# Performance work log

Hardware: AMD Instinct MI355X
Metric: run time of the kernel (lower is better)

The kernel has to match this reference:

```python
import jax, jax.numpy as jnp
import numpy as np


def setup_inputs() -> dict:
    key = jax.random.key(0)
    k1, k2, k3, k4 = jax.random.split(key, 4)
    B, H, W, C = 4, 64, 64, 512
    x = jax.random.normal(k1, (B, H, W, C), dtype=jnp.float32)
    Wb = jax.random.normal(k2, (C, C // 8), dtype=jnp.float32) * 0.05
    Wc = jax.random.normal(k3, (C, C // 8), dtype=jnp.float32) * 0.05
    Wd = jax.random.normal(k4, (C, C), dtype=jnp.float32) * 0.05
    gamma = jnp.ones((1,), dtype=jnp.float32)
    return {"x": x, "Wb": Wb, "Wc": Wc, "Wd": Wd, "gamma": gamma}


def reference(x, Wb, Wc, Wd, gamma):
    B, H, W, C = x.shape
    hw = H * W
    xf = x.reshape(B, hw, C)                      # [B, hw, C]
    b = jnp.einsum('bnc,ck->bnk', xf, Wb)         # key   [B, hw, C/8]
    c = jnp.einsum('bnc,ck->bnk', xf, Wc)         # query [B, hw, C/8]
    d = jnp.einsum('bnc,cf->bnf', xf, Wd)         # value [B, hw, C]
    # attention energy: c @ b^T, softmax over last axis (keras default)
    energy = jnp.einsum('bqk,bnk->bqn', c, b)     # [B, hw, hw]
    attn = jax.nn.softmax(energy, axis=-1)
    out = jnp.einsum('bqn,bnf->bqf', attn, d)     # [B, hw, C]
    out = out.reshape(B, H, W, C)
    return gamma * out + x
```

## Files before the change

kernel.cpp:

```cpp
#include <hip/hip_runtime.h>
#include <hip/hip_bf16.h>
#include <stdint.h>

typedef __attribute__((ext_vector_type(8))) short short8;
typedef __attribute__((ext_vector_type(4))) float f32x4;
typedef _Float16 half8 __attribute__((ext_vector_type(8)));

#define LOG2E 1.4426950408889634f
#define SHIFT2 100.98865286222744f

__device__ __forceinline__ unsigned short f2bf(float f) {
  union { float f; unsigned u; } v; v.f = f;
  unsigned u = v.u;
  unsigned r = u + 0x7FFF + ((u >> 16) & 1);
  return (unsigned short)(r >> 16);
}
__device__ __forceinline__ float bf2f(unsigned short h) {
  union { unsigned u; float f; } v; v.u = ((unsigned)h) << 16; return v.f;
}

__global__ void convert_x_kernel(const float* __restrict__ x,
                                 unsigned short* __restrict__ xh,
                                 _Float16* __restrict__ xf, int n4) {
  int i = blockIdx.x * blockDim.x + threadIdx.x;
  if (i >= n4) return;
  float4 v = ((const float4*)x)[i];
  ushort4 h;
  h.x = f2bf(v.x); h.y = f2bf(v.y); h.z = f2bf(v.z); h.w = f2bf(v.w);
  union { _Float16 f[4]; ushort4 u; } p;
  p.f[0] = (_Float16)v.x; p.f[1] = (_Float16)v.y;
  p.f[2] = (_Float16)v.z; p.f[3] = (_Float16)v.w;
  ((ushort4*)xh)[i] = h;
  ((ushort4*)xf)[i] = p.u;
}

__global__ void prep_w_kernel(const float* __restrict__ Wb,
                              const float* __restrict__ Wc,
                              const float* __restrict__ Wd,
                              _Float16* __restrict__ wf,
                              unsigned short* __restrict__ whd) {
  int gid = blockIdx.x * 256 + threadIdx.x;
  int n = gid >> 9, k = gid & 511;
  if (n < 128) {
    float v = (n < 64) ? Wb[k * 64 + n] : Wc[k * 64 + (n - 64)];
    wf[n * 512 + k] = (_Float16)v;
  } else {
    whd[(size_t)(n - 128) * 512 + k] = f2bf(Wd[k * 512 + (n - 128)]);
  }
}

__launch_bounds__(256)
__global__ void proj_gemm_kernel(const unsigned short* __restrict__ xh,
                                 const _Float16* __restrict__ xf,
                                 const unsigned short* __restrict__ whd,
                                 const _Float16* __restrict__ wf,
                                 _Float16* __restrict__ bq,
                                 _Float16* __restrict__ cq,
                                 unsigned short* __restrict__ dT) {
  __shared__ unsigned short As[128 * 32];
  __shared__ unsigned short Bs[128 * 32];
  const int row0 = blockIdx.x * 128;
  const int col0 = blockIdx.y * 128;
  const bool bc = (blockIdx.y == 0);
  const int w = threadIdx.x >> 6;
  const int lane = threadIdx.x & 63;
  const int wm = (w >> 1) * 64, wn = (w & 1) * 64;
  const int quad = lane >> 4, m16 = lane & 15;
  const int lrow = lane >> 2, lseg = lane & 3;

  const unsigned short* asrc = bc ? (const unsigned short*)xf : xh;
  const unsigned short* bsrc = bc ? (const unsigned short*)wf : whd;
  const int bcol0 = bc ? 0 : (col0 - 128);

  const f32x4 fzero = {0.f, 0.f, 0.f, 0.f};
  f32x4 acc[4][4];
  for (int i = 0; i < 4; i++)
    for (int j = 0; j < 4; j++) acc[i][j] = fzero;

  for (int k0 = 0; k0 < 512; k0 += 32) {
    for (int i = 0; i < 2; i++) {
      int r = (w * 2 + i) * 16 + lrow;
      size_t aoff = (size_t)(row0 + r) * 512 + k0 + lseg * 8;
      size_t boff = (size_t)(bcol0 + r) * 512 + k0 + lseg * 8;
      int loff = r * 32 + lseg * 8;
      __builtin_amdgcn_global_load_lds(
          (const __attribute__((address_space(1))) unsigned int*)(asrc + aoff),
          (__attribute__((address_space(3))) unsigned int*)(As + loff), 16, 0, 0);
      __builtin_amdgcn_global_load_lds(
          (const __attribute__((address_space(1))) unsigned int*)(bsrc + boff),
          (__attribute__((address_space(3))) unsigned int*)(Bs + loff), 16, 0, 0);
    }
    __syncthreads();
    if (bc) {
      half8 ah[4], bh[4];
      for (int mt = 0; mt < 4; mt++)
        ah[mt] = *(const half8*)(As + (wm + mt * 16 + m16) * 32 + quad * 8);
      for (int nt = 0; nt < 4; nt++)
        bh[nt] = *(const half8*)(Bs + (wn + nt * 16 + m16) * 32 + quad * 8);
      for (int mt = 0; mt < 4; mt++)
        for (int nt = 0; nt < 4; nt++)
          acc[mt][nt] = __builtin_amdgcn_mfma_f32_16x16x32_f16(ah[mt], bh[nt],
                                                               acc[mt][nt], 0, 0, 0);
    } else {
      short8 ah[4], bh[4];
      for (int mt = 0; mt < 4; mt++)
        ah[mt] = *(const short8*)(As + (wm + mt * 16 + m16) * 32 + quad * 8);
      for (int nt = 0; nt < 4; nt++)
        bh[nt] = *(const short8*)(Bs + (wn + nt * 16 + m16) * 32 + quad * 8);
      for (int mt = 0; mt < 4; mt++)
        for (int nt = 0; nt < 4; nt++)
          acc[mt][nt] = __builtin_amdgcn_mfma_f32_16x16x32_bf16(ah[mt], bh[nt],
                                                                acc[mt][nt], 0, 0, 0);
    }
    __syncthreads();
  }

  for (int mt = 0; mt < 4; mt++) {
    int rowb = row0 + wm + mt * 16 + quad * 4;
    for (int nt = 0; nt < 4; nt++) {
      int n = wn + nt * 16 + m16;
      f32x4 v = acc[mt][nt];
      if (bc) {
        _Float16* dst = (n < 64) ? bq : cq;
        int nn = n & 63;
        for (int r = 0; r < 4; r++)
          dst[(size_t)(rowb + r) * 64 + nn] = (_Float16)v[r];
      } else {
        int f = col0 - 128 + n;
        int batch = rowb >> 12, tok = rowb & 4095;
        ushort4 o;
        o.x = f2bf(v[0]); o.y = f2bf(v[1]); o.z = f2bf(v[2]); o.w = f2bf(v[3]);
        *(ushort4*)(dT + ((size_t)batch * 512 + f) * 4096 + tok) = o;
      }
    }
  }
}

#define PSTR 72

__launch_bounds__(256, 2)
__global__ void attn_kernel(const _Float16* __restrict__ bq,
                            const _Float16* __restrict__ cq,
                            const unsigned short* __restrict__ dT,
                            float* __restrict__ O0,
                            float* __restrict__ O1,
                            float* __restrict__ lbuf) {
  __shared__ unsigned short p_lds[2][64 * PSTR];

  const int batch = blockIdx.y;
  const int split = blockIdx.z;
  const int q0 = blockIdx.x * 64;
  const int tid = threadIdx.x;
  const int w = tid >> 6, lane = tid & 63;
  const int quad = lane >> 4, m16 = lane & 15;
  const int colc = w * 16 + m16;

  const _Float16* cb = cq + ((size_t)batch * 4096 + q0) * 64;
  const _Float16* kb = bq + (size_t)batch * 4096 * 64;
  const unsigned short* vb = dT + (size_t)batch * 512 * 4096;
  float* Op = split ? O1 : O0;

  half8 qf[4][2];
  for (int mt = 0; mt < 4; mt++)
    for (int ks = 0; ks < 2; ks++)
      qf[mt][ks] = *(const half8*)(cb + (size_t)(mt * 16 + m16) * 64 +
                                   ks * 32 + quad * 8);

  const f32x4 fzero = {0.f, 0.f, 0.f, 0.f};
  f32x4 acc[4][8];
  for (int i = 0; i < 4; i++)
    for (int j = 0; j < 8; j++) acc[i][j] = fzero;

  const int sq = tid >> 2, sseg = tid & 3;
  float psum = 0.0f;

  const int kt0 = split * 32, kt1 = kt0 + 32;

  auto qk_step = [&](int kti, int nbuf) {
    const _Float16* kp = kb + ((size_t)kti * 64 + colc) * 64 + quad * 8;
    half8 K0 = *(const half8*)(kp);
    half8 K1 = *(const half8*)(kp + 32);
    for (int mt = 0; mt < 4; mt++) {
      f32x4 s = __builtin_amdgcn_mfma_f32_16x16x32_f16(qf[mt][0], K0, fzero, 0, 0, 0);
      s = __builtin_amdgcn_mfma_f32_16x16x32_f16(qf[mt][1], K1, s, 0, 0, 0);
      int rbase = mt * 16 + quad * 4;
#pragma unroll
      for (int r = 0; r < 4; r++) {
        float p = __builtin_amdgcn_exp2f(fmaf(s[r], LOG2E, -SHIFT2));
        p_lds[nbuf][(rbase + r) * PSTR + colc] = f2bf(p);
      }
    }
  };

  qk_step(kt0, 0);
  __syncthreads();

  for (int kt = kt0; kt < kt1; kt++) {
    const int buf = kt & 1;

    short8 vf0[8];
#pragma unroll
    for (int ft = 0; ft < 8; ft++)
      vf0[ft] = *(const short8*)(vb + (size_t)(w * 128 + ft * 16 + m16) * 4096 +
                                 kt * 64 + quad * 8);

    if (kt + 1 < kt1) qk_step(kt + 1, buf ^ 1);

    short8 vf1[8];
#pragma unroll
    for (int ft = 0; ft < 8; ft++)
      vf1[ft] = *(const short8*)(vb + (size_t)(w * 128 + ft * 16 + m16) * 4096 +
                                 kt * 64 + 32 + quad * 8);

    {
      const unsigned short* pr = p_lds[buf] + sq * PSTR + sseg * 16;
      short8 a = *(const short8*)(pr);
      short8 b = *(const short8*)(pr + 8);
      float ps = 0.f;
#pragma unroll
      for (int i = 0; i < 8; i++)
        ps += bf2f((unsigned short)a[i]) + bf2f((unsigned short)b[i]);
      psum += ps;
    }

    for (int ks = 0; ks < 2; ks++) {
      short8 pf[4];
      for (int mt = 0; mt < 4; mt++)
        pf[mt] = *(const short8*)(p_lds[buf] + (mt * 16 + m16) * PSTR +
                                  ks * 32 + quad * 8);
      const short8* vv = ks ? vf1 : vf0;
      for (int ft = 0; ft < 8; ft++)
        for (int mt = 0; mt < 4; mt++)
          acc[mt][ft] = __builtin_amdgcn_mfma_f32_16x16x32_bf16(pf[mt], vv[ft],
                                                                acc[mt][ft], 0, 0, 0);
    }
    __syncthreads();
  }

  psum += __shfl_xor(psum, 1);
  psum += __shfl_xor(psum, 2);
  if (sseg == 0)
    lbuf[(size_t)split * 16384 + batch * 4096 + (q0 + sq)] = psum;
  for (int mt = 0; mt < 4; mt++) {
    for (int ft = 0; ft < 8; ft++) {
      int f = w * 128 + ft * 16 + m16;
      for (int r = 0; r < 4; r++) {
        int row = q0 + mt * 16 + quad * 4 + r;
        Op[((size_t)batch * 4096 + row) * 512 + f] = acc[mt][ft][r];
      }
    }
  }
}

__global__ void combine_kernel(const float* __restrict__ O0,
                               const float* __restrict__ O1,
                               const float* __restrict__ lbuf,
                               const float* __restrict__ x,
                               const float* __restrict__ gamma,
                               float* __restrict__ out) {
  int gid = blockIdx.x * 256 + threadIdx.x;
  int row = gid >> 7;
  float rl = 1.0f / (lbuf[row] + lbuf[16384 + row]);
  float g = gamma[0];
  float4 o0 = ((const float4*)O0)[gid];
  float4 o1 = ((const float4*)O1)[gid];
  float4 xv = ((const float4*)x)[gid];
  float4 r;
  r.x = g * ((o0.x + o1.x) * rl) + xv.x;
  r.y = g * ((o0.y + o1.y) * rl) + xv.y;
  r.z = g * ((o0.z + o1.z) * rl) + xv.z;
  r.w = g * ((o0.w + o1.w) * rl) + xv.w;
  ((float4*)out)[gid] = r;
}

extern "C" void kernel_launch(void* const* d_in, const int* in_sizes, int n_in,
                              void* d_out, int out_size, void* d_ws, size_t ws_size,
                              hipStream_t stream) {
  (void)in_sizes; (void)n_in; (void)out_size; (void)ws_size;
  const float* x = (const float*)d_in[0];
  const float* Wb = (const float*)d_in[1];
  const float* Wc = (const float*)d_in[2];
  const float* Wd = (const float*)d_in[3];
  const float* gamma = (const float*)d_in[4];
  float* out = (float*)d_out;

  unsigned short* ws = (unsigned short*)d_ws;
  unsigned short* xh  = ws;
  _Float16* xf  = (_Float16*)(ws + 8388608);
  unsigned short* whd = ws + 16777216;
  _Float16* wf  = (_Float16*)(ws + 17039360);
  _Float16* bqp = (_Float16*)(ws + 17104896);
  _Float16* cqp = (_Float16*)(ws + 18153472);
  unsigned short* dT  = ws + 19202048;
  float* lb = (float*)(ws + 27590656);
  float* Opart0 = out;
  float* Opart1 = (float*)ws;

  convert_x_kernel<<<8192, 256, 0, stream>>>(x, xh, xf, 2097152);
  prep_w_kernel<<<1280, 256, 0, stream>>>(Wb, Wc, Wd, wf, whd);
  proj_gemm_kernel<<<dim3(128, 5), 256, 0, stream>>>(xh, xf, whd, wf,
                                                     bqp, cqp, dT);
  attn_kernel<<<dim3(64, 4, 2), 256, 0, stream>>>(bqp, cqp, dT,
                                                  Opart0, Opart1, lb);
  combine_kernel<<<8192, 256, 0, stream>>>(Opart0, Opart1, lb, x, gamma, out);
}
```

Measured before the change: 295.8 us.

## Double key tile to 128 per iteration and software-pipeline V loads with PV MFMAs

Each loop iteration now handles 128 keys instead of 64. The P tile in LDS widens to match, which halves the number of barriers. V fragments are ping-pong loaded into two register sets and interleaved with four PV MFMA sub-steps, so global loads overlap compute. The PV MFMAs are wrapped in s_setprio, and the barrier is replaced by an explicit lgkmcnt wait plus s_barrier. The cost is more register pressure and more LDS, which may hurt occupancy at 2 blocks/CU.

```diff
diff --git a/kernel.cpp b/kernel.cpp
--- a/kernel.cpp
+++ b/kernel.cpp
@@ -136,7 +136,7 @@
   }
 }
 
-#define PSTR 72
+#define PSTR 136
 
 __launch_bounds__(256, 2)
 __global__ void attn_kernel(const _Float16* __restrict__ bq,
@@ -174,67 +174,99 @@
   const int sq = tid >> 2, sseg = tid & 3;
   float psum = 0.0f;
 
-  const int kt0 = split * 32, kt1 = kt0 + 32;
-
-  auto qk_step = [&](int kti, int nbuf) {
-    const _Float16* kp = kb + ((size_t)kti * 64 + colc) * 64 + quad * 8;
-    half8 K0 = *(const half8*)(kp);
-    half8 K1 = *(const half8*)(kp + 32);
+  const int kB0 = split * 2048;
+
+  auto qk_compute = [&](int kbase, int nbuf) {
+    const _Float16* kp0 = kb + (size_t)(kbase + colc) * 64 + quad * 8;
+    const _Float16* kp1 = kp0 + (size_t)64 * 64;
+    half8 K00 = *(const half8*)(kp0);
+    half8 K01 = *(const half8*)(kp0 + 32);
+    half8 K10 = *(const half8*)(kp1);
+    half8 K11 = *(const half8*)(kp1 + 32);
+#pragma unroll
     for (int mt = 0; mt < 4; mt++) {
-      f32x4 s = __builtin_amdgcn_mfma_f32_16x16x32_f16(qf[mt][0], K0, fzero, 0, 0, 0);
-      s = __builtin_amdgcn_mfma_f32_16x16x32_f16(qf[mt][1], K1, s, 0, 0, 0);
+      f32x4 s0 = __builtin_amdgcn_mfma_f32_16x16x32_f16(qf[mt][0], K00, fzero, 0, 0, 0);
+      s0 = __builtin_amdgcn_mfma_f32_16x16x32_f16(qf[mt][1], K01, s0, 0, 0, 0);
+      f32x4 s1 = __builtin_amdgcn_mfma_f32_16x16x32_f16(qf[mt][0], K10, fzero, 0, 0, 0);
+      s1 = __builtin_amdgcn_mfma_f32_16x16x32_f16(qf[mt][1], K11, s1, 0, 0, 0);
       int rbase = mt * 16 + quad * 4;
 #pragma unroll
       for (int r = 0; r < 4; r++) {
-        float p = __builtin_amdgcn_exp2f(fmaf(s[r], LOG2E, -SHIFT2));
-        p_lds[nbuf][(rbase + r) * PSTR + colc] = f2bf(p);
+        float p0 = __builtin_amdgcn_exp2f(fmaf(s0[r], LOG2E, -SHIFT2));
+        float p1 = __builtin_amdgcn_exp2f(fmaf(s1[r], LOG2E, -SHIFT2));
+        p_lds[nbuf][(rbase + r) * PSTR + colc] = f2bf(p0);
+        p_lds[nbuf][(rbase + r) * PSTR + 64 + colc] = f2bf(p1);
       }
     }
   };
 
-  qk_step(kt0, 0);
-  __syncthreads();
-
-  for (int kt = kt0; kt < kt1; kt++) {
-    const int buf = kt & 1;
-
-    short8 vf0[8];
+  auto vload = [&](short8* dst, int koff) {
 #pragma unroll
     for (int ft = 0; ft < 8; ft++)
-      vf0[ft] = *(const short8*)(vb + (size_t)(w * 128 + ft * 16 + m16) * 4096 +
-                                 kt * 64 + quad * 8);
-
-    if (kt + 1 < kt1) qk_step(kt + 1, buf ^ 1);
-
-    short8 vf1[8];
+      dst[ft] = *(const short8*)(vb + (size_t)(w * 128 + ft * 16 + m16) * 4096 +
+                                 koff + quad * 8);
+  };
+
+  auto pv_step = [&](int buf, int ks, const short8* vv) {
+    short8 pf[4];
+#pragma unroll
+    for (int mt = 0; mt < 4; mt++)
+      pf[mt] = *(const short8*)(p_lds[buf] + (mt * 16 + m16) * PSTR +
+                                ks * 32 + quad * 8);
+    __builtin_amdgcn_s_setprio(1);
 #pragma unroll
     for (int ft = 0; ft < 8; ft++)
-      vf1[ft] = *(const short8*)(vb + (size_t)(w * 128 + ft * 16 + m16) * 4096 +
-                                 kt * 64 + 32 + quad * 8);
+#pragma unroll
+      for (int mt = 0; mt < 4; mt++)
+        acc[mt][ft] = __builtin_amdgcn_mfma_f32_16x16x32_bf16(pf[mt], vv[ft],
+                                                              acc[mt][ft], 0, 0, 0);
+    __builtin_amdgcn_s_setprio(0);
+  };
+
+#define BARRIER()                                          \
+  do {                                                     \
+    asm volatile("s_waitcnt lgkmcnt(0)" ::: "memory");     \
+    __builtin_amdgcn_s_barrier();                          \
+    asm volatile("" ::: "memory");                         \
+  } while (0)
+
+  short8 vfA[8], vfB[8];
+
+  qk_compute(kB0, 0);
+  vload(vfA, kB0);
+  BARRIER();
+
+  for (int it = 0; it < 16; ++it) {
+    const int buf = it & 1;
+    const int kbase = kB0 + it * 128;
+
+    vload(vfB, kbase + 32);
+
+    if (it < 15) qk_compute(kbase + 128, buf ^ 1);
 
     {
-      const unsigned short* pr = p_lds[buf] + sq * PSTR + sseg * 16;
+      const unsigned short* pr = p_lds[buf] + sq * PSTR + sseg * 32;
       short8 a = *(const short8*)(pr);
       short8 b = *(const short8*)(pr + 8);
+      short8 c = *(const short8*)(pr + 16);
+      short8 d = *(const short8*)(pr + 24);
       float ps = 0.f;
 #pragma unroll
       for (int i = 0; i < 8; i++)
-        ps += bf2f((unsigned short)a[i]) + bf2f((unsigned short)b[i]);
+        ps += (bf2f((unsigned short)a[i]) + bf2f((unsigned short)b[i])) +
+              (bf2f((unsigned short)c[i]) + bf2f((unsigned short)d[i]));
       psum += ps;
     }
 
-    for (int ks = 0; ks < 2; ks++) {
-      short8 pf[4];
-      for (int mt = 0; mt < 4; mt++)
-        pf[mt] = *(const short8*)(p_lds[buf] + (mt * 16 + m16) * PSTR +
-                                  ks * 32 + quad * 8);
-      const short8* vv = ks ? vf1 : vf0;
-      for (int ft = 0; ft < 8; ft++)
-        for (int mt = 0; mt < 4; mt++)
-          acc[mt][ft] = __builtin_amdgcn_mfma_f32_16x16x32_bf16(pf[mt], vv[ft],
-                                                                acc[mt][ft], 0, 0, 0);
-    }
-    __syncthreads();
+    pv_step(buf, 0, vfA);
+    vload(vfA, kbase + 64);
+    pv_step(buf, 1, vfB);
+    vload(vfB, kbase + 96);
+    pv_step(buf, 2, vfA);
+    pv_step(buf, 3, vfB);
+    if (it < 15) vload(vfA, kbase + 128);
+
+    BARRIER();
   }
 
   psum += __shfl_xor(psum, 1);
```

New measurement: 317.0 us. +7.2%, slower.

## Use 128-query tiles with 512 threads, XCD-aware mapping, and a register-pipelined K/V prefetch

Applied to the files above, without the earlier changes.

The attention kernel now runs 512-thread blocks covering 128 queries, split into two query groups of four waves each, so every loaded V tile feeds twice as many rows. The grid becomes a flat 256 blocks whose low three bits pick batch and split, intended to keep each batch/split on one XCD for L2 locality. K loads are double-buffered in registers two steps ahead, V loads are interleaved between the two PV halves, and s_setprio is raised around the MFMA bursts. The cost is more LDS per block, more register pressure under launch_bounds(512,2), and only 256 blocks, which may not fill the GPU well.

```diff
diff --git a/kernel.cpp b/kernel.cpp
--- a/kernel.cpp
+++ b/kernel.cpp
@@ -137,33 +137,40 @@
 }
 
 #define PSTR 72
-
-__launch_bounds__(256, 2)
+#define NT 32
+
+__launch_bounds__(512, 2)
 __global__ void attn_kernel(const _Float16* __restrict__ bq,
                             const _Float16* __restrict__ cq,
                             const unsigned short* __restrict__ dT,
                             float* __restrict__ O0,
                             float* __restrict__ O1,
                             float* __restrict__ lbuf) {
-  __shared__ unsigned short p_lds[2][64 * PSTR];
-
-  const int batch = blockIdx.y;
-  const int split = blockIdx.z;
-  const int q0 = blockIdx.x * 64;
+  __shared__ unsigned short p_lds[2][128 * PSTR];
+
+  const int flat = blockIdx.x;
+  const int xcd = flat & 7;
+  const int batch = xcd >> 1;
+  const int split = xcd & 1;
+  const int q0 = (flat >> 3) * 128;
+
   const int tid = threadIdx.x;
   const int w = tid >> 6, lane = tid & 63;
+  const int qg = w >> 2, fw = w & 3;
   const int quad = lane >> 4, m16 = lane & 15;
-  const int colc = w * 16 + m16;
+  const int colc = fw * 16 + m16;
 
   const _Float16* cb = cq + ((size_t)batch * 4096 + q0) * 64;
-  const _Float16* kb = bq + (size_t)batch * 4096 * 64;
-  const unsigned short* vb = dT + (size_t)batch * 512 * 4096;
+  const _Float16* kb = bq + ((size_t)batch * 4096 + split * 2048) * 64;
+  const unsigned short* vb = dT + (size_t)batch * 512 * 4096 + split * 2048;
   float* Op = split ? O1 : O0;
 
   half8 qf[4][2];
+#pragma unroll
   for (int mt = 0; mt < 4; mt++)
+#pragma unroll
     for (int ks = 0; ks < 2; ks++)
-      qf[mt][ks] = *(const half8*)(cb + (size_t)(mt * 16 + m16) * 64 +
+      qf[mt][ks] = *(const half8*)(cb + (size_t)(qg * 64 + mt * 16 + m16) * 64 +
                                    ks * 32 + quad * 8);
 
   const f32x4 fzero = {0.f, 0.f, 0.f, 0.f};
@@ -174,16 +181,18 @@
   const int sq = tid >> 2, sseg = tid & 3;
   float psum = 0.0f;
 
-  const int kt0 = split * 32, kt1 = kt0 + 32;
-
-  auto qk_step = [&](int kti, int nbuf) {
-    const _Float16* kp = kb + ((size_t)kti * 64 + colc) * 64 + quad * 8;
-    half8 K0 = *(const half8*)(kp);
-    half8 K1 = *(const half8*)(kp + 32);
+  auto kload = [&](half8& K0, half8& K1, int t) {
+    const _Float16* kp = kb + (size_t)(t * 64 + colc) * 64 + quad * 8;
+    K0 = *(const half8*)(kp);
+    K1 = *(const half8*)(kp + 32);
+  };
+
+  auto qk_compute = [&](int nbuf, const half8& K0, const half8& K1) {
+#pragma unroll
     for (int mt = 0; mt < 4; mt++) {
       f32x4 s = __builtin_amdgcn_mfma_f32_16x16x32_f16(qf[mt][0], K0, fzero, 0, 0, 0);
       s = __builtin_amdgcn_mfma_f32_16x16x32_f16(qf[mt][1], K1, s, 0, 0, 0);
-      int rbase = mt * 16 + quad * 4;
+      int rbase = qg * 64 + mt * 16 + quad * 4;
 #pragma unroll
       for (int r = 0; r < 4; r++) {
         float p = __builtin_amdgcn_exp2f(fmaf(s[r], LOG2E, -SHIFT2));
@@ -192,25 +201,49 @@
     }
   };
 
-  qk_step(kt0, 0);
-  __syncthreads();
-
-  for (int kt = kt0; kt < kt1; kt++) {
-    const int buf = kt & 1;
-
-    short8 vf0[8];
+  auto vload = [&](short8* dst, int koff) {
 #pragma unroll
     for (int ft = 0; ft < 8; ft++)
-      vf0[ft] = *(const short8*)(vb + (size_t)(w * 128 + ft * 16 + m16) * 4096 +
-                                 kt * 64 + quad * 8);
-
-    if (kt + 1 < kt1) qk_step(kt + 1, buf ^ 1);
-
-    short8 vf1[8];
+      dst[ft] = *(const short8*)(vb + (size_t)(fw * 128 + ft * 16 + m16) * 4096 +
+                                 koff + quad * 8);
+  };
+
+  auto pv_step = [&](int buf, int ks, const short8* vv) {
+    short8 pf[4];
+#pragma unroll
+    for (int mt = 0; mt < 4; mt++)
+      pf[mt] = *(const short8*)(p_lds[buf] + (qg * 64 + mt * 16 + m16) * PSTR +
+                                ks * 32 + quad * 8);
+    __builtin_amdgcn_s_setprio(1);
 #pragma unroll
     for (int ft = 0; ft < 8; ft++)
-      vf1[ft] = *(const short8*)(vb + (size_t)(w * 128 + ft * 16 + m16) * 4096 +
-                                 kt * 64 + 32 + quad * 8);
+#pragma unroll
+      for (int mt = 0; mt < 4; mt++)
+        acc[mt][ft] = __builtin_amdgcn_mfma_f32_16x16x32_bf16(pf[mt], vv[ft],
+                                                              acc[mt][ft], 0, 0, 0);
+    __builtin_amdgcn_s_setprio(0);
+  };
+
+#define BARRIER()                                          \
+  do {                                                     \
+    asm volatile("s_waitcnt lgkmcnt(0)" ::: "memory");     \
+    __builtin_amdgcn_s_barrier();                          \
+    asm volatile("" ::: "memory");                         \
+  } while (0)
+
+  short8 vfA[8];
+  half8 KA0, KA1, KB0, KB1;
+
+  vload(vfA, 0);
+  kload(KA0, KA1, 0);
+  qk_compute(0, KA0, KA1);
+  kload(KB0, KB1, 1);
+  BARRIER();
+
+  auto iter = [&](int it, int buf, half8& Kc0, half8& Kc1,
+                  half8& Kn0, half8& Kn1) {
+    if (it + 1 < NT) qk_compute(buf ^ 1, Kc0, Kc1);
+    if (it + 2 < NT) kload(Kn0, Kn1, it + 2);
 
     {
       const unsigned short* pr = p_lds[buf] + sq * PSTR + sseg * 16;
@@ -223,18 +256,17 @@
       psum += ps;
     }
 
-    for (int ks = 0; ks < 2; ks++) {
-      short8 pf[4];
-      for (int mt = 0; mt < 4; mt++)
-        pf[mt] = *(const short8*)(p_lds[buf] + (mt * 16 + m16) * PSTR +
-                                  ks * 32 + quad * 8);
-      const short8* vv = ks ? vf1 : vf0;
-      for (int ft = 0; ft < 8; ft++)
-        for (int mt = 0; mt < 4; mt++)
-          acc[mt][ft] = __builtin_amdgcn_mfma_f32_16x16x32_bf16(pf[mt], vv[ft],
-                                                                acc[mt][ft], 0, 0, 0);
-    }
-    __syncthreads();
+    pv_step(buf, 0, vfA);
+    vload(vfA, it * 64 + 32);
+    pv_step(buf, 1, vfA);
+    if (it + 1 < NT) vload(vfA, (it + 1) * 64);
+
+    BARRIER();
+  };
+
+  for (int it = 0; it < NT; it += 2) {
+    iter(it, 0, KB0, KB1, KA0, KA1);
+    iter(it + 1, 1, KA0, KA1, KB0, KB1);
   }
 
   psum += __shfl_xor(psum, 1);
@@ -243,9 +275,9 @@
     lbuf[(size_t)split * 16384 + batch * 4096 + (q0 + sq)] = psum;
   for (int mt = 0; mt < 4; mt++) {
     for (int ft = 0; ft < 8; ft++) {
-      int f = w * 128 + ft * 16 + m16;
+      int f = fw * 128 + ft * 16 + m16;
       for (int r = 0; r < 4; r++) {
-        int row = q0 + mt * 16 + quad * 4 + r;
+        int row = q0 + qg * 64 + mt * 16 + quad * 4 + r;
         Op[((size_t)batch * 4096 + row) * 512 + f] = acc[mt][ft][r];
       }
     }
@@ -300,7 +332,6 @@
   prep_w_kernel<<<1280, 256, 0, stream>>>(Wb, Wc, Wd, wf, whd);
   proj_gemm_kernel<<<dim3(128, 5), 256, 0, stream>>>(xh, xf, whd, wf,
                                                      bqp, cqp, dT);
-  attn_kernel<<<dim3(64, 4, 2), 256, 0, stream>>>(bqp, cqp, dT,
-                                                  Opart0, Opart1, lb);
+  attn_kernel<<<256, 512, 0, stream>>>(bqp, cqp, dT, Opart0, Opart1, lb);
   combine_kernel<<<8192, 256, 0, stream>>>(Opart0, Opart1, lb, x, gamma, out);
 }
```

Measured after the change: 413.5 us. +39.8%, slower.

## Compute full P tile per wave to drop block barriers in attention loop

Applied to the files above, without the earlier changes.

Each wave now computes the whole 64x64 score tile itself using swapped MFMA operands, so P is transposed into per-wave LDS and no __syncthreads is needed inside the key loop. Row sums are accumulated in registers from the fp32 exponentials instead of re-reading bf16 P from LDS, and MFMA issue priority is raised around the PV block. The cost is fourfold redundant QK^T and exp work per block, a larger LDS footprint, and the loss of the explicit QK/PV prefetch overlap.

```diff
diff --git a/kernel.cpp b/kernel.cpp
--- a/kernel.cpp
+++ b/kernel.cpp
@@ -145,7 +145,7 @@
                             float* __restrict__ O0,
                             float* __restrict__ O1,
                             float* __restrict__ lbuf) {
-  __shared__ unsigned short p_lds[2][64 * PSTR];
+  __shared__ unsigned short p_lds[4][64 * PSTR];
 
   const int batch = blockIdx.y;
   const int split = blockIdx.z;
@@ -153,15 +153,17 @@
   const int tid = threadIdx.x;
   const int w = tid >> 6, lane = tid & 63;
   const int quad = lane >> 4, m16 = lane & 15;
-  const int colc = w * 16 + m16;
 
   const _Float16* cb = cq + ((size_t)batch * 4096 + q0) * 64;
-  const _Float16* kb = bq + (size_t)batch * 4096 * 64;
-  const unsigned short* vb = dT + (size_t)batch * 512 * 4096;
+  const _Float16* kb = bq + ((size_t)batch * 4096 + split * 2048) * 64;
+  const unsigned short* vb = dT + (size_t)batch * 512 * 4096 + split * 2048;
   float* Op = split ? O1 : O0;
+  unsigned short* pb = &p_lds[w][0];
 
   half8 qf[4][2];
+#pragma unroll
   for (int mt = 0; mt < 4; mt++)
+#pragma unroll
     for (int ks = 0; ks < 2; ks++)
       qf[mt][ks] = *(const half8*)(cb + (size_t)(mt * 16 + m16) * 64 +
                                    ks * 32 + quad * 8);
@@ -171,76 +173,87 @@
   for (int i = 0; i < 4; i++)
     for (int j = 0; j < 8; j++) acc[i][j] = fzero;
 
-  const int sq = tid >> 2, sseg = tid & 3;
-  float psum = 0.0f;
-
-  const int kt0 = split * 32, kt1 = kt0 + 32;
-
-  auto qk_step = [&](int kti, int nbuf) {
-    const _Float16* kp = kb + ((size_t)kti * 64 + colc) * 64 + quad * 8;
-    half8 K0 = *(const half8*)(kp);
-    half8 K1 = *(const half8*)(kp + 32);
+  float psum[4] = {0.f, 0.f, 0.f, 0.f};
+
+  auto qk_half = [&](int kbase, int h) {
+    const _Float16* kp = kb + (size_t)(kbase + h * 32 + m16) * 64 + quad * 8;
+    half8 KA0 = *(const half8*)(kp);
+    half8 KA1 = *(const half8*)(kp + 32);
+    half8 KB0 = *(const half8*)(kp + 16 * 64);
+    half8 KB1 = *(const half8*)(kp + 16 * 64 + 32);
+#pragma unroll
     for (int mt = 0; mt < 4; mt++) {
-      f32x4 s = __builtin_amdgcn_mfma_f32_16x16x32_f16(qf[mt][0], K0, fzero, 0, 0, 0);
-      s = __builtin_amdgcn_mfma_f32_16x16x32_f16(qf[mt][1], K1, s, 0, 0, 0);
-      int rbase = mt * 16 + quad * 4;
-#pragma unroll
-      for (int r = 0; r < 4; r++) {
-        float p = __builtin_amdgcn_exp2f(fmaf(s[r], LOG2E, -SHIFT2));
-        p_lds[nbuf][(rbase + r) * PSTR + colc] = f2bf(p);
-      }
+      f32x4 sA = __builtin_amdgcn_mfma_f32_16x16x32_f16(KA0, qf[mt][0], fzero, 0, 0, 0);
+      sA = __builtin_amdgcn_mfma_f32_16x16x32_f16(KA1, qf[mt][1], sA, 0, 0, 0);
+      f32x4 sB = __builtin_amdgcn_mfma_f32_16x16x32_f16(KB0, qf[mt][0], fzero, 0, 0, 0);
+      sB = __builtin_amdgcn_mfma_f32_16x16x32_f16(KB1, qf[mt][1], sB, 0, 0, 0);
+      float pa0 = __builtin_amdgcn_exp2f(fmaf(sA[0], LOG2E, -SHIFT2));
+      float pa1 = __builtin_amdgcn_exp2f(fmaf(sA[1], LOG2E, -SHIFT2));
+      float pa2 = __builtin_amdgcn_exp2f(fmaf(sA[2], LOG2E, -SHIFT2));
+      float pa3 = __builtin_amdgcn_exp2f(fmaf(sA[3], LOG2E, -SHIFT2));
+      float pb0 = __builtin_amdgcn_exp2f(fmaf(sB[0], LOG2E, -SHIFT2));
+      float pb1 = __builtin_amdgcn_exp2f(fmaf(sB[1], LOG2E, -SHIFT2));
+      float pb2 = __builtin_amdgcn_exp2f(fmaf(sB[2], LOG2E, -SHIFT2));
+      float pb3 = __builtin_amdgcn_exp2f(fmaf(sB[3], LOG2E, -SHIFT2));
+      psum[mt] += ((pa0 + pa1) + (pa2 + pa3)) + ((pb0 + pb1) + (pb2 + pb3));
+      uint2 wa, wb2;
+      wa.x = ((unsigned)f2bf(pa1) << 16) | f2bf(pa0);
+      wa.y = ((unsigned)f2bf(pa3) << 16) | f2bf(pa2);
+      wb2.x = ((unsigned)f2bf(pb1) << 16) | f2bf(pb0);
+      wb2.y = ((unsigned)f2bf(pb3) << 16) | f2bf(pb2);
+      int rowoff = (mt * 16 + m16) * PSTR + quad * 4 + h * 32;
+      *(uint2*)(pb + rowoff) = wa;
+      *(uint2*)(pb + rowoff + 16) = wb2;
     }
   };
 
-  qk_step(kt0, 0);
-  __syncthreads();
-
-  for (int kt = kt0; kt < kt1; kt++) {
-    const int buf = kt & 1;
-
-    short8 vf0[8];
+  auto vload = [&](short8* dst, int koff) {
 #pragma unroll
     for (int ft = 0; ft < 8; ft++)
-      vf0[ft] = *(const short8*)(vb + (size_t)(w * 128 + ft * 16 + m16) * 4096 +
-                                 kt * 64 + quad * 8);
-
-    if (kt + 1 < kt1) qk_step(kt + 1, buf ^ 1);
-
-    short8 vf1[8];
+      dst[ft] = *(const short8*)(vb + (size_t)(w * 128 + ft * 16 + m16) * 4096 +
+                                 koff + quad * 8);
+  };
+
+  auto pv_step = [&](int ks, const short8* vv) {
+    short8 pf[4];
+#pragma unroll
+    for (int mt = 0; mt < 4; mt++)
+      pf[mt] = *(const short8*)(pb + (mt * 16 + m16) * PSTR +
+                                ks * 32 + quad * 8);
+    __builtin_amdgcn_s_setprio(1);
 #pragma unroll
     for (int ft = 0; ft < 8; ft++)
-      vf1[ft] = *(const short8*)(vb + (size_t)(w * 128 + ft * 16 + m16) * 4096 +
-                                 kt * 64 + 32 + quad * 8);
-
-    {
-      const unsigned short* pr = p_lds[buf] + sq * PSTR + sseg * 16;
-      short8 a = *(const short8*)(pr);
-      short8 b = *(const short8*)(pr + 8);
-      float ps = 0.f;
-#pragma unroll
-      for (int i = 0; i < 8; i++)
-        ps += bf2f((unsigned short)a[i]) + bf2f((unsigned short)b[i]);
-      psum += ps;
-    }
-
-    for (int ks = 0; ks < 2; ks++) {
-      short8 pf[4];
-      for (int mt = 0; mt < 4; mt++)
-        pf[mt] = *(const short8*)(p_lds[buf] + (mt * 16 + m16) * PSTR +
-                                  ks * 32 + quad * 8);
-      const short8* vv = ks ? vf1 : vf0;
-      for (int ft = 0; ft < 8; ft++)
-        for (int mt = 0; mt < 4; mt++)
-          acc[mt][ft] = __builtin_amdgcn_mfma_f32_16x16x32_bf16(pf[mt], vv[ft],
-                                                                acc[mt][ft], 0, 0, 0);
-    }
-    __syncthreads();
-  }
-
-  psum += __shfl_xor(psum, 1);
-  psum += __shfl_xor(psum, 2);
-  if (sseg == 0)
-    lbuf[(size_t)split * 16384 + batch * 4096 + (q0 + sq)] = psum;
+#pragma unroll
+      for (int mt = 0; mt < 4; mt++)
+        acc[mt][ft] = __builtin_amdgcn_mfma_f32_16x16x32_bf16(pf[mt], vv[ft],
+                                                              acc[mt][ft], 0, 0, 0);
+    __builtin_amdgcn_s_setprio(0);
+  };
+
+  short8 vf[8];
+
+  for (int kt = 0; kt < 32; ++kt) {
+    const int kbase = kt * 64;
+    vload(vf, kbase);
+    qk_half(kbase, 0);
+    qk_half(kbase, 1);
+    pv_step(0, vf);
+    vload(vf, kbase + 32);
+    pv_step(1, vf);
+  }
+
+#pragma unroll
+  for (int mt = 0; mt < 4; mt++) {
+    psum[mt] += __shfl_xor(psum[mt], 16);
+    psum[mt] += __shfl_xor(psum[mt], 32);
+  }
+  if (w == 0 && quad == 0) {
+#pragma unroll
+    for (int mt = 0; mt < 4; mt++)
+      lbuf[(size_t)split * 16384 + batch * 4096 + (q0 + mt * 16 + m16)] =
+          psum[mt];
+  }
+
   for (int mt = 0; mt < 4; mt++) {
     for (int ft = 0; ft < 8; ft++) {
       int f = w * 128 + ft * 16 + m16;
```

New measurement: 483.3 us. 63.4% more time.
